# Performance work log

Hardware: AMD Instinct MI355X
Metric: run time of the kernel (lower is better)

Reference implementation:

```python
import jax, jax.numpy as jnp
import numpy as np


def setup_inputs() -> dict:
    key = jax.random.key(0)
    kx, kw = jax.random.split(key)
    x = jax.random.normal(kx, (32, 128, 8192), dtype=jnp.float32)
    weight = jax.random.normal(kw, (128, 128, 1, 2), dtype=jnp.float32)
    return {"x": x, "weight": weight}


def reference(x, weight):
    # x: (bs, cin, d); weight: (cout, cin, 1, 2)
    bs, cin, d = x.shape
    xp = x.reshape(bs, cin, d // 2, 2)          # (bs, cin, d/2, 2)
    w = weight[:, :, 0, :]                      # (cout, cin, 2)
    # out[b, o, p] = sum_{c,k} x[b,c,p,k] * w[o,c,k] / sqrt(cin)
    out = jnp.einsum('bcpk,ock->bop', xp, w) / jnp.sqrt(jnp.float32(cin))
    return out
```

## Files before the change

kernel.cpp:

```cpp
#include <hip/hip_runtime.h>
#include <stdint.h>


typedef __attribute__((ext_vector_type(8))) short bf16x8;
typedef __attribute__((ext_vector_type(4))) float f32x4;

#define CIN  128
#define DLEN 8192
#define PLEN 4096
#define COUT 128

__device__ inline unsigned short f2bf(float f) {
    unsigned u = __builtin_bit_cast(unsigned, f);
    unsigned r = u + 0x7FFFu + ((u >> 16) & 1u);
    return (unsigned short)(r >> 16);
}

__global__ __launch_bounds__(256) void convert_w(const float* __restrict__ w,
                                                 unsigned short* __restrict__ wb) {
    int t  = blockIdx.x * 256 + threadIdx.x;
    int o  = t >> 7;
    int k0 = (t & 127) * 2;
    const float scale = 0.088388347648318447f;
    float2 f = *(const float2*)(w + o * 256 + k0);
    unsigned v = (unsigned)f2bf(f.x * scale) | ((unsigned)f2bf(f.y * scale) << 16);
    int idx = (k0 >> 3) * 1024 + o * 8 + (k0 & 7);
    *(unsigned*)(wb + idx) = v;
}

__global__ __launch_bounds__(256, 3) void conv_mfma(const float* __restrict__ x,
                                                    const unsigned short* __restrict__ wb,
                                                    float* __restrict__ out) {
    int tile = blockIdx.x;
    int b    = tile >> 5;
    int pt   = (tile & 31) * 128;
    int lane = threadIdx.x & 63;
    int w    = threadIdx.x >> 6;
    int quad = lane >> 4;
    int l16  = lane & 15;

    const float* xb = x + (size_t)b * ((size_t)CIN * DLEN);
    int p0 = pt + w * 32 + l16;

    f32x4 acc[2][8];
#pragma unroll
    for (int mt = 0; mt < 2; ++mt)
#pragma unroll
        for (int t = 0; t < 8; ++t)
            acc[mt][t] = (f32x4)(0.0f);

    const uint32_t* wb32 = (const uint32_t*)wb;

#pragma unroll 1
    for (int kc = 0; kc < 8; ++kc) {
        int cbase = kc * 16 + quad * 4;
        float2 af0[4], af1[4];
#pragma unroll
        for (int jj = 0; jj < 4; ++jj) {
            const float* rowp = xb + (size_t)(cbase + jj) * DLEN + 2 * p0;
            af0[jj] = *(const float2*)(rowp);
            af1[jj] = *(const float2*)(rowp + 32);
        }
        union { bf16x8 v; unsigned uu[4]; } afr0, afr1;
#pragma unroll
        for (int jj = 0; jj < 4; ++jj) {
            afr0.uu[jj] = (unsigned)f2bf(af0[jj].x) | ((unsigned)f2bf(af0[jj].y) << 16);
            afr1.uu[jj] = (unsigned)f2bf(af1[jj].x) | ((unsigned)f2bf(af1[jj].y) << 16);
        }

        const uint32_t* bbase = wb32 + (size_t)(kc * 4 + quad) * 512 + l16 * 4;
#pragma unroll
        for (int t = 0; t < 8; ++t) {
            union { bf16x8 v; uint4 u; } bf_;
            bf_.u = *(const uint4*)(bbase + t * 64);
            acc[0][t] = __builtin_amdgcn_mfma_f32_16x16x32_bf16(afr0.v, bf_.v, acc[0][t], 0, 0, 0);
            acc[1][t] = __builtin_amdgcn_mfma_f32_16x16x32_bf16(afr1.v, bf_.v, acc[1][t], 0, 0, 0);
        }
    }

    float* ob = out + (size_t)b * ((size_t)COUT * PLEN);
#pragma unroll
    for (int t = 0; t < 8; ++t) {
        int o = t * 16 + l16;
        float* orow = ob + (size_t)o * PLEN + pt + w * 32 + quad * 4;
        *(f32x4*)(orow)      = acc[0][t];
        *(f32x4*)(orow + 16) = acc[1][t];
    }
}

extern "C" void kernel_launch(void* const* d_in, const int* in_sizes, int n_in,
                              void* d_out, int out_size, void* d_ws, size_t ws_size,
                              hipStream_t stream) {
    const float* x = (const float*)d_in[0];
    const float* w = (const float*)d_in[1];
    float* out = (float*)d_out;
    unsigned short* wb = (unsigned short*)d_ws;

    convert_w<<<64, 256, 0, stream>>>(w, wb);
    conv_mfma<<<1024, 256, 0, stream>>>(x, wb, out);
}
```

Before: 219.2 us.

## Prefetch next x chunk with float4 loads and remap positions to interleave outputs

Each lane now loads one float4 (four consecutive x values) per row instead of two float2 loads, so its two M-tiles cover adjacent positions. The output store is remapped to interleave them. The next K-chunk's x loads are issued before the current chunk's MFMAs, giving a register double-buffer that hides global latency, and weight loads are batched in groups of four. Launch bounds raise target occupancy to 4 blocks per CU, which adds register pressure and a possible spill risk.

```diff
diff --git a/kernel.cpp b/kernel.cpp
--- a/kernel.cpp
+++ b/kernel.cpp
@@ -16,6 +16,14 @@
     return (unsigned short)(r >> 16);
 }
 
+__device__ inline unsigned pack_bf(float a, float b) {
+    unsigned ua = __builtin_bit_cast(unsigned, a);
+    unsigned ub = __builtin_bit_cast(unsigned, b);
+    unsigned ra = ua + 0x7FFFu + ((ua >> 16) & 1u);
+    unsigned rb = ub + 0x7FFFu + ((ub >> 16) & 1u);
+    return (ra >> 16) | (rb & 0xFFFF0000u);
+}
+
 __global__ __launch_bounds__(256) void convert_w(const float* __restrict__ w,
                                                  unsigned short* __restrict__ wb) {
     int t  = blockIdx.x * 256 + threadIdx.x;
@@ -28,7 +36,7 @@
     *(unsigned*)(wb + idx) = v;
 }
 
-__global__ __launch_bounds__(256, 3) void conv_mfma(const float* __restrict__ x,
+__global__ __launch_bounds__(256, 4) void conv_mfma(const float* __restrict__ x,
                                                     const unsigned short* __restrict__ wb,
                                                     float* __restrict__ out) {
     int tile = blockIdx.x;
@@ -38,9 +46,11 @@
     int w    = threadIdx.x >> 6;
     int quad = lane >> 4;
     int l16  = lane & 15;
+    int pbase = pt + w * 32;
 
-    const float* xb = x + (size_t)b * ((size_t)CIN * DLEN);
-    int p0 = pt + w * 32 + l16;
+    const float* xl = x + (size_t)b * ((size_t)CIN * DLEN)
+                        + (size_t)(quad * 4) * DLEN + 2 * pbase + 4 * l16;
+    const uint32_t* bb = (const uint32_t*)wb + quad * 512 + l16 * 4;
 
     f32x4 acc[2][8];
 #pragma unroll
@@ -49,42 +59,50 @@
         for (int t = 0; t < 8; ++t)
             acc[mt][t] = (f32x4)(0.0f);
 
-    const uint32_t* wb32 = (const uint32_t*)wb;
+    float4 abuf[4];
+#pragma unroll
+    for (int jj = 0; jj < 4; ++jj)
+        abuf[jj] = *(const float4*)(xl + (size_t)jj * DLEN);
 
 #pragma unroll 1
     for (int kc = 0; kc < 8; ++kc) {
-        int cbase = kc * 16 + quad * 4;
-        float2 af0[4], af1[4];
-#pragma unroll
-        for (int jj = 0; jj < 4; ++jj) {
-            const float* rowp = xb + (size_t)(cbase + jj) * DLEN + 2 * p0;
-            af0[jj] = *(const float2*)(rowp);
-            af1[jj] = *(const float2*)(rowp + 32);
-        }
         union { bf16x8 v; unsigned uu[4]; } afr0, afr1;
 #pragma unroll
         for (int jj = 0; jj < 4; ++jj) {
-            afr0.uu[jj] = (unsigned)f2bf(af0[jj].x) | ((unsigned)f2bf(af0[jj].y) << 16);
-            afr1.uu[jj] = (unsigned)f2bf(af1[jj].x) | ((unsigned)f2bf(af1[jj].y) << 16);
+            afr0.uu[jj] = pack_bf(abuf[jj].x, abuf[jj].y);
+            afr1.uu[jj] = pack_bf(abuf[jj].z, abuf[jj].w);
         }
-
-        const uint32_t* bbase = wb32 + (size_t)(kc * 4 + quad) * 512 + l16 * 4;
+        if (kc < 7) {
+            const float* nx = xl + (size_t)((kc + 1) * 16) * DLEN;
 #pragma unroll
-        for (int t = 0; t < 8; ++t) {
-            union { bf16x8 v; uint4 u; } bf_;
-            bf_.u = *(const uint4*)(bbase + t * 64);
-            acc[0][t] = __builtin_amdgcn_mfma_f32_16x16x32_bf16(afr0.v, bf_.v, acc[0][t], 0, 0, 0);
-            acc[1][t] = __builtin_amdgcn_mfma_f32_16x16x32_bf16(afr1.v, bf_.v, acc[1][t], 0, 0, 0);
+            for (int jj = 0; jj < 4; ++jj)
+                abuf[jj] = *(const float4*)(nx + (size_t)jj * DLEN);
+        }
+        const uint32_t* bk = bb + kc * 2048;
+#pragma unroll
+        for (int th = 0; th < 2; ++th) {
+            union { bf16x8 v; uint4 u; } bfr[4];
+#pragma unroll
+            for (int tt = 0; tt < 4; ++tt)
+                bfr[tt].u = *(const uint4*)(bk + (th * 4 + tt) * 64);
+#pragma unroll
+            for (int tt = 0; tt < 4; ++tt) {
+                int t = th * 4 + tt;
+                acc[0][t] = __builtin_amdgcn_mfma_f32_16x16x32_bf16(afr0.v, bfr[tt].v, acc[0][t], 0, 0, 0);
+                acc[1][t] = __builtin_amdgcn_mfma_f32_16x16x32_bf16(afr1.v, bfr[tt].v, acc[1][t], 0, 0, 0);
+            }
         }
     }
 
-    float* ob = out + (size_t)b * ((size_t)COUT * PLEN);
+    float* ob = out + (size_t)b * ((size_t)COUT * PLEN) + pbase + quad * 8;
 #pragma unroll
     for (int t = 0; t < 8; ++t) {
         int o = t * 16 + l16;
-        float* orow = ob + (size_t)o * PLEN + pt + w * 32 + quad * 4;
-        *(f32x4*)(orow)      = acc[0][t];
-        *(f32x4*)(orow + 16) = acc[1][t];
+        float* orow = ob + (size_t)o * PLEN;
+        f32x4 v0 = { acc[0][t][0], acc[1][t][0], acc[0][t][1], acc[1][t][1] };
+        f32x4 v1 = { acc[0][t][2], acc[1][t][2], acc[0][t][3], acc[1][t][3] };
+        *(f32x4*)(orow)     = v0;
+        *(f32x4*)(orow + 4) = v1;
     }
 }
 
```

After: 212.7 us. 2.9% less time.
